# Performance work log

Measured on AMD Instinct MI355X. Metric: run time of the kernel, lower is better.

## Reference

```python
import jax, jax.numpy as jnp
import numpy as np

NUM_EMBEDDINGS = 2048
EMBEDDING_DIM = 64
COMMITMENT_COST = 0.25


def setup_inputs() -> dict:
    key = jax.random.key(0)
    k_z, k_w = jax.random.split(key)
    z = jax.random.normal(k_z, (32, EMBEDDING_DIM, 64, 64), dtype=jnp.float32)
    # torch init: uniform(-1/K, 1/K)
    embedding_w = jax.random.uniform(
        k_w, (NUM_EMBEDDINGS, EMBEDDING_DIM), dtype=jnp.float32,
        minval=-1.0 / NUM_EMBEDDINGS, maxval=1.0 / NUM_EMBEDDINGS)
    return {"z": z, "embedding_w": embedding_w}


def reference(z, embedding_w):
    # z: (B, C, H, W), C == embedding_dim
    B, C, H, W = z.shape
    zp = jnp.transpose(z, (0, 2, 3, 1))          # (B, H, W, C)
    zf = zp.reshape(-1, C)                        # (N, C)
    # squared L2 distance to every codebook entry: (N, K)
    d = (jnp.sum(zf * zf, axis=1, keepdims=True)
         + jnp.sum(embedding_w * embedding_w, axis=1)
         - 2.0 * jnp.matmul(zf, embedding_w.T))
    indices = jnp.argmin(d, axis=1)               # (N,) int
    quantized = embedding_w[indices].reshape(zp.shape)  # (B, H, W, C)
    # training-mode commitment loss: cc * mse(stop_grad(q), z)
    loss = COMMITMENT_COST * jnp.mean(
        (jax.lax.stop_gradient(quantized) - zp) ** 2)
    # straight-through estimator
    quantized_st = zp + jax.lax.stop_gradient(quantized - zp)
    quantized_out = jnp.transpose(quantized_st, (0, 3, 1, 2))  # (B, C, H, W)
    return quantized_out, indices.reshape(B, H, W), loss
```

## Files before the change

kernel.cpp:

```cpp
#include <hip/hip_runtime.h>


#define KCODES   2048
#define CDIM     64
#define OUT_Q    0
#define OUT_IDX  8388608
#define OUT_LOSS 8519680
#define ZSTR     72
#define CAP      32
#define B_MAX    1.6e-5f

typedef float f2    __attribute__((ext_vector_type(2)));
typedef float f32x4 __attribute__((ext_vector_type(4)));
typedef short s16x8 __attribute__((ext_vector_type(8)));
typedef unsigned long long u64;
typedef unsigned short u16;
typedef unsigned int u32;

__device__ __forceinline__ u16 f2bf(float x) {
    u32 u = __float_as_uint(x);
    return (u16)((u + 0x7fffu + ((u >> 16) & 1u)) >> 16);
}
__device__ __forceinline__ u32 encf(float f) {
    u32 b = __float_as_uint(f);
    return (b & 0x80000000u) ? ~b : (b | 0x80000000u);
}
__device__ __forceinline__ float decf(u32 e) {
    return __uint_as_float((e & 0x80000000u) ? (e ^ 0x80000000u) : ~e);
}

__device__ __forceinline__ float fc(const float4& v, int i) {
    return i == 0 ? v.x : (i == 1 ? v.y : (i == 2 ? v.z : v.w));
}

__device__ __forceinline__ float pairwise64(const float a[64]) {
    float r[8];
#pragma unroll
    for (int j = 0; j < 8; ++j) r[j] = a[j];
#pragma unroll
    for (int m = 1; m < 8; ++m)
#pragma unroll
        for (int j = 0; j < 8; ++j) r[j] = __fadd_rn(r[j], a[m * 8 + j]);
    float s01 = __fadd_rn(r[0], r[1]);
    float s23 = __fadd_rn(r[2], r[3]);
    float s45 = __fadd_rn(r[4], r[5]);
    float s67 = __fadd_rn(r[6], r[7]);
    return __fadd_rn(__fadd_rn(s01, s23), __fadd_rn(s45, s67));
}

__device__ __forceinline__ float exact_d(const float* __restrict__ zp,
                                         const float* __restrict__ wk,
                                         float Sr, float bk) {
    float acc = 0.f;
#pragma unroll
    for (int c0 = 0; c0 < 64; c0 += 4) {
        const float4 wc = *(const float4*)(wk + c0);
        acc = __builtin_fmaf(zp[(size_t)(c0 + 0) * 4096], wc.x, acc);
        acc = __builtin_fmaf(zp[(size_t)(c0 + 1) * 4096], wc.y, acc);
        acc = __builtin_fmaf(zp[(size_t)(c0 + 2) * 4096], wc.z, acc);
        acc = __builtin_fmaf(zp[(size_t)(c0 + 3) * 4096], wc.w, acc);
    }
    float Sb = __fadd_rn(Sr, bk);
    return __builtin_fmaf(acc, -2.0f, Sb);
}

__global__ __launch_bounds__(256) void vq_bsum(const float* __restrict__ w,
                                               float* __restrict__ bsum,
                                               u16* __restrict__ wf0,
                                               u16* __restrict__ wf1) {
    int k = blockIdx.x * 256 + threadIdx.x;
    const float4* wr = (const float4*)(w + (size_t)k * CDIM);
    float4 v[16];
    float a[64];
#pragma unroll
    for (int m = 0; m < 16; ++m) {
        v[m] = wr[m];
        a[4 * m + 0] = __fmul_rn(v[m].x, v[m].x);
        a[4 * m + 1] = __fmul_rn(v[m].y, v[m].y);
        a[4 * m + 2] = __fmul_rn(v[m].z, v[m].z);
        a[4 * m + 3] = __fmul_rn(v[m].w, v[m].w);
    }
    bsum[k] = pairwise64(a);

    const int g = k >> 4, i16 = k & 15;
#pragma unroll
    for (int h = 0; h < 2; ++h) {
        u16* wf = h ? wf1 : wf0;
#pragma unroll
        for (int o = 0; o < 4; ++o) {
            float4 va = v[h * 8 + o * 2];
            float4 vb = v[h * 8 + o * 2 + 1];
            u64 p0 = (u64)f2bf(va.x) | ((u64)f2bf(va.y) << 16)
                   | ((u64)f2bf(va.z) << 32) | ((u64)f2bf(va.w) << 48);
            u64 p1 = (u64)f2bf(vb.x) | ((u64)f2bf(vb.y) << 16)
                   | ((u64)f2bf(vb.z) << 32) | ((u64)f2bf(vb.w) << 48);
            u64* dst = (u64*)(wf + (size_t)(g * 64 + o * 16 + i16) * 8);
            dst[0] = p0; dst[1] = p1;
        }
    }
}

__global__ __launch_bounds__(256, 4) void vq_main(const float* __restrict__ z,
                                                  const float* __restrict__ w,
                                                  const float* __restrict__ bsum,
                                                  const u16* __restrict__ wf0,
                                                  const u16* __restrict__ wf1,
                                                  float* __restrict__ out,
                                                  double* __restrict__ partial) {
    __shared__ u16 zsh[64 * ZSTR];
    __shared__ float Ssh[64];
    __shared__ u32 rowmin[64];
    __shared__ float thr[64];
    __shared__ u64 skey[64];
    __shared__ u32 cnt[64];
    __shared__ u16 cand[64][CAP];
    __shared__ double lredd[4];

    const int t  = threadIdx.x;
    const int l  = t & 63;
    const int wv = t >> 6;
    const int bb = blockIdx.x;
    const size_t zbase = (size_t)(bb >> 6) * 262144 + (size_t)(bb & 63) * 64;

    if (t < 64) {
        skey[t]   = 0xFFFFFFFFFFFFFFFFull;
        cnt[t]    = 0u;
        rowmin[t] = 0xFFFFFFFFu;
    }

#pragma unroll
    for (int m = 0; m < 8; ++m) {
        int i = m * 256 + t;
        int p = i & 31;
        int c = i >> 5;
        f2 v = *(const f2*)(z + zbase + (size_t)c * 4096 + 2 * p);
        zsh[(2 * p)     * ZSTR + c] = f2bf(v.x);
        zsh[(2 * p + 1) * ZSTR + c] = f2bf(v.y);
    }

    if (t < 64) {
        const float* zp = z + zbase + t;
        float r[8];
#pragma unroll
        for (int j = 0; j < 8; ++j) {
            float v = zp[(size_t)j * 4096];
            r[j] = __fmul_rn(v, v);
        }
#pragma unroll
        for (int m = 1; m < 8; ++m)
#pragma unroll
            for (int j = 0; j < 8; ++j) {
                float v = zp[(size_t)(m * 8 + j) * 4096];
                r[j] = __fadd_rn(r[j], __fmul_rn(v, v));
            }
        float s01 = __fadd_rn(r[0], r[1]);
        float s23 = __fadd_rn(r[2], r[3]);
        float s45 = __fadd_rn(r[4], r[5]);
        float s67 = __fadd_rn(r[6], r[7]);
        Ssh[t] = __fadd_rn(__fadd_rn(s01, s23), __fadd_rn(s45, s67));
    }
    __syncthreads();

    s16x8 afrag[4][2];
#pragma unroll
    for (int mt = 0; mt < 4; ++mt)
#pragma unroll
        for (int kb = 0; kb < 2; ++kb)
            afrag[mt][kb] = *(const s16x8*)&zsh[(mt * 16 + (l & 15)) * ZSTR
                                               + kb * 32 + (l >> 4) * 8];

    const int gbase = __builtin_amdgcn_readfirstlane(wv) * 32;

    float rmin[4][4];
#pragma unroll
    for (int mt = 0; mt < 4; ++mt)
#pragma unroll
        for (int rg = 0; rg < 4; ++rg) rmin[mt][rg] = __builtin_inff();

    {
        s16x8 nb0 = *(const s16x8*)(wf0 + (size_t)(gbase * 64 + l) * 8);
        s16x8 nb1 = *(const s16x8*)(wf1 + (size_t)(gbase * 64 + l) * 8);
        float nbv = bsum[gbase * 16 + (l & 15)];
        for (int g2 = 0; g2 < 32; ++g2) {
            s16x8 b0 = nb0, b1 = nb1;
            float bv = nbv;
            if (g2 < 31) {
                int gn = gbase + g2 + 1;
                nb0 = *(const s16x8*)(wf0 + (size_t)(gn * 64 + l) * 8);
                nb1 = *(const s16x8*)(wf1 + (size_t)(gn * 64 + l) * 8);
                nbv = bsum[gn * 16 + (l & 15)];
            }
#pragma unroll
            for (int mt = 0; mt < 4; ++mt) {
                f32x4 acc = {0.f, 0.f, 0.f, 0.f};
                acc = __builtin_amdgcn_mfma_f32_16x16x32_bf16(afrag[mt][0], b0, acc, 0, 0, 0);
                acc = __builtin_amdgcn_mfma_f32_16x16x32_bf16(afrag[mt][1], b1, acc, 0, 0, 0);
#pragma unroll
                for (int rg = 0; rg < 4; ++rg) {
                    float v = __builtin_fmaf(acc[rg], -2.0f, bv);
                    rmin[mt][rg] = fminf(rmin[mt][rg], v);
                }
            }
        }
    }

#pragma unroll
    for (int mt = 0; mt < 4; ++mt)
#pragma unroll
        for (int rg = 0; rg < 4; ++rg) {
            float m = rmin[mt][rg];
            m = fminf(m, __shfl_xor(m, 1, 64));
            m = fminf(m, __shfl_xor(m, 2, 64));
            m = fminf(m, __shfl_xor(m, 4, 64));
            m = fminf(m, __shfl_xor(m, 8, 64));
            if ((l & 15) == 0)
                atomicMin(&rowmin[mt * 16 + (l >> 4) * 4 + rg], encf(m));
        }
    __syncthreads();

    if (t < 64) {
        float S = Ssh[t];
        thr[t] = decf(rowmin[t])
               + (0.03125f * sqrtf(S * B_MAX) + 7.6294e-6f * (S + 1.0f));
    }
    __syncthreads();

    float thrr[4][4];
#pragma unroll
    for (int mt = 0; mt < 4; ++mt)
#pragma unroll
        for (int rg = 0; rg < 4; ++rg)
            thrr[mt][rg] = thr[mt * 16 + (l >> 4) * 4 + rg];

    {
        s16x8 nb0 = *(const s16x8*)(wf0 + (size_t)(gbase * 64 + l) * 8);
        s16x8 nb1 = *(const s16x8*)(wf1 + (size_t)(gbase * 64 + l) * 8);
        float nbv = bsum[gbase * 16 + (l & 15)];
        for (int g2 = 0; g2 < 32; ++g2) {
            const int g = gbase + g2;
            s16x8 b0 = nb0, b1 = nb1;
            float bv = nbv;
            if (g2 < 31) {
                int gn = g + 1;
                nb0 = *(const s16x8*)(wf0 + (size_t)(gn * 64 + l) * 8);
                nb1 = *(const s16x8*)(wf1 + (size_t)(gn * 64 + l) * 8);
                nbv = bsum[gn * 16 + (l & 15)];
            }
#pragma unroll
            for (int mt = 0; mt < 4; ++mt) {
                f32x4 acc = {0.f, 0.f, 0.f, 0.f};
                acc = __builtin_amdgcn_mfma_f32_16x16x32_bf16(afrag[mt][0], b0, acc, 0, 0, 0);
                acc = __builtin_amdgcn_mfma_f32_16x16x32_bf16(afrag[mt][1], b1, acc, 0, 0, 0);
#pragma unroll
                for (int rg = 0; rg < 4; ++rg) {
                    float v = __builtin_fmaf(acc[rg], -2.0f, bv);
                    if (v <= thrr[mt][rg]) {
                        int row = mt * 16 + (l >> 4) * 4 + rg;
                        u32 pos = atomicAdd(&cnt[row], 1u);
                        if (pos < CAP)
                            cand[row][pos] = (u16)(g * 16 + (l & 15));
                    }
                }
            }
        }
    }
    __syncthreads();

    {
        const int row  = t & 63;
        const int part = t >> 6;
        const float* zp = z + zbase + row;
        const float Sr = Ssh[row];
        u32 n = cnt[row];
        if (n <= CAP) {
            for (u32 i = part; i < n; i += 4) {
                int k = cand[row][i];
                float d = exact_d(zp, w + (size_t)k * CDIM, Sr, bsum[k]);
                atomicMin(&skey[row], ((u64)__float_as_uint(d) << 32) | (u64)(u32)k);
            }
        } else {
            for (int k = part; k < KCODES; k += 4) {
                float d = exact_d(zp, w + (size_t)k * CDIM, Sr, bsum[k]);
                atomicMin(&skey[row], ((u64)__float_as_uint(d) << 32) | (u64)(u32)k);
            }
        }
    }
    __syncthreads();

    {
        const int row = l;
        const u32 kq = (u32)(skey[row] & 0xFFFFFFFFull);
        if (wv == 0) out[OUT_IDX + (size_t)bb * 64 + row] = (float)kq;

        const float* wq = w + (size_t)kq * CDIM + wv * 16;
        const float* zp = z + zbase + row;
        double lacc = 0.0;
#pragma unroll
        for (int c4 = 0; c4 < 16; c4 += 4) {
            const float4 q4 = *(const float4*)(wq + c4);
#pragma unroll
            for (int i = 0; i < 4; ++i) {
                int c = wv * 16 + c4 + i;
                float zv = zp[(size_t)c * 4096];
                float d1  = __fsub_rn(fc(q4, i), zv);
                float val = __fadd_rn(zv, d1);
                out[OUT_Q + zbase + (size_t)c * 4096 + row] = val;
                lacc += (double)__fmul_rn(d1, d1);
            }
        }
#pragma unroll
        for (int off = 1; off < 64; off <<= 1) lacc += __shfl_xor(lacc, off, 64);
        if (l == 0) lredd[wv] = lacc;
    }
    __syncthreads();
    if (t == 0) partial[bb] = lredd[0] + lredd[1] + lredd[2] + lredd[3];
}

__global__ __launch_bounds__(256) void vq_loss(const double* __restrict__ partial,
                                               float* __restrict__ out) {
    int t = threadIdx.x;
    double s = 0.0;
#pragma unroll
    for (int i = 0; i < 8; ++i) s += partial[t + i * 256];
#pragma unroll
    for (int off = 1; off < 64; off <<= 1) s += __shfl_xor(s, off, 64);
    __shared__ double sr[4];
    if ((t & 63) == 0) sr[t >> 6] = s;
    __syncthreads();
    if (t == 0)
        out[OUT_LOSS] = (float)((sr[0] + sr[1] + sr[2] + sr[3]) * (0.25 / 8388608.0));
}

extern "C" void kernel_launch(void* const* d_in, const int* in_sizes, int n_in,
                              void* d_out, int out_size, void* d_ws, size_t ws_size,
                              hipStream_t stream) {
    (void)in_sizes; (void)n_in; (void)out_size; (void)ws_size;
    const float* z = (const float*)d_in[0];
    const float* w = (const float*)d_in[1];
    float* out     = (float*)d_out;

    float*  bsum    = (float*)d_ws;
    u16*    wf0     = (u16*)((char*)d_ws + 8192);
    u16*    wf1     = (u16*)((char*)d_ws + 8192 + 131072);
    double* partial = (double*)((char*)d_ws + 8192 + 262144);

    vq_bsum<<<8, 256, 0, stream>>>(w, bsum, wf0, wf1);
    vq_main<<<2048, 256, 0, stream>>>(z, w, bsum, wf0, wf1, out, partial);
    vq_loss<<<1, 256, 0, stream>>>(partial, out);
}
```

Baseline: 190.0 us.

## Halve rows per block to 32 and fold -2 scale and bias into MFMA

Each block now handles 32 spatial rows instead of 64, so twice as many blocks are launched and every block streams the full bf16 codebook for half as many rows. The z fragments are pre-scaled by -2 and the MFMA accumulator is seeded with the codebook norm, which removes the per-element FMA before the min and threshold checks. The candidate-rescoring and output stages are remapped to 8 parts per row. The change trades codebook reuse per block (twice the codebook traffic from cache) for more parallelism and lower register use. The -2 scaling before bf16 rounding is exact and leaves the filter bounds unchanged.

```diff
diff --git a/kernel.cpp b/kernel.cpp
--- a/kernel.cpp
+++ b/kernel.cpp
@@ -7,6 +7,7 @@
 #define OUT_IDX  8388608
 #define OUT_LOSS 8519680
 #define ZSTR     72
+#define BR       32
 #define CAP      32
 #define B_MAX    1.6e-5f
 
@@ -107,38 +108,38 @@
                                                   const u16* __restrict__ wf1,
                                                   float* __restrict__ out,
                                                   double* __restrict__ partial) {
-    __shared__ u16 zsh[64 * ZSTR];
-    __shared__ float Ssh[64];
-    __shared__ u32 rowmin[64];
-    __shared__ float thr[64];
-    __shared__ u64 skey[64];
-    __shared__ u32 cnt[64];
-    __shared__ u16 cand[64][CAP];
+    __shared__ u16 zsh[BR * ZSTR];
+    __shared__ float Ssh[BR];
+    __shared__ u32 rowmin[BR];
+    __shared__ float thr[BR];
+    __shared__ u64 skey[BR];
+    __shared__ u32 cnt[BR];
+    __shared__ u16 cand[BR][CAP];
     __shared__ double lredd[4];
 
     const int t  = threadIdx.x;
     const int l  = t & 63;
     const int wv = t >> 6;
     const int bb = blockIdx.x;
-    const size_t zbase = (size_t)(bb >> 6) * 262144 + (size_t)(bb & 63) * 64;
-
-    if (t < 64) {
+    const size_t zbase = (size_t)(bb >> 7) * 262144 + (size_t)(bb & 127) * 32;
+
+    if (t < BR) {
         skey[t]   = 0xFFFFFFFFFFFFFFFFull;
         cnt[t]    = 0u;
         rowmin[t] = 0xFFFFFFFFu;
     }
 
 #pragma unroll
-    for (int m = 0; m < 8; ++m) {
+    for (int m = 0; m < 4; ++m) {
         int i = m * 256 + t;
-        int p = i & 31;
-        int c = i >> 5;
+        int p = i & 15;
+        int c = i >> 4;
         f2 v = *(const f2*)(z + zbase + (size_t)c * 4096 + 2 * p);
-        zsh[(2 * p)     * ZSTR + c] = f2bf(v.x);
-        zsh[(2 * p + 1) * ZSTR + c] = f2bf(v.y);
-    }
-
-    if (t < 64) {
+        zsh[(2 * p)     * ZSTR + c] = f2bf(-2.0f * v.x);
+        zsh[(2 * p + 1) * ZSTR + c] = f2bf(-2.0f * v.y);
+    }
+
+    if (t < BR) {
         const float* zp = z + zbase + t;
         float r[8];
 #pragma unroll
@@ -161,9 +162,9 @@
     }
     __syncthreads();
 
-    s16x8 afrag[4][2];
-#pragma unroll
-    for (int mt = 0; mt < 4; ++mt)
+    s16x8 afrag[2][2];
+#pragma unroll
+    for (int mt = 0; mt < 2; ++mt)
 #pragma unroll
         for (int kb = 0; kb < 2; ++kb)
             afrag[mt][kb] = *(const s16x8*)&zsh[(mt * 16 + (l & 15)) * ZSTR
@@ -171,9 +172,9 @@
 
     const int gbase = __builtin_amdgcn_readfirstlane(wv) * 32;
 
-    float rmin[4][4];
-#pragma unroll
-    for (int mt = 0; mt < 4; ++mt)
+    float rmin[2][4];
+#pragma unroll
+    for (int mt = 0; mt < 2; ++mt)
 #pragma unroll
         for (int rg = 0; rg < 4; ++rg) rmin[mt][rg] = __builtin_inff();
 
@@ -191,21 +192,19 @@
                 nbv = bsum[gn * 16 + (l & 15)];
             }
 #pragma unroll
-            for (int mt = 0; mt < 4; ++mt) {
-                f32x4 acc = {0.f, 0.f, 0.f, 0.f};
+            for (int mt = 0; mt < 2; ++mt) {
+                f32x4 acc = {bv, bv, bv, bv};
                 acc = __builtin_amdgcn_mfma_f32_16x16x32_bf16(afrag[mt][0], b0, acc, 0, 0, 0);
                 acc = __builtin_amdgcn_mfma_f32_16x16x32_bf16(afrag[mt][1], b1, acc, 0, 0, 0);
 #pragma unroll
-                for (int rg = 0; rg < 4; ++rg) {
-                    float v = __builtin_fmaf(acc[rg], -2.0f, bv);
-                    rmin[mt][rg] = fminf(rmin[mt][rg], v);
-                }
-            }
-        }
-    }
-
-#pragma unroll
-    for (int mt = 0; mt < 4; ++mt)
+                for (int rg = 0; rg < 4; ++rg)
+                    rmin[mt][rg] = fminf(rmin[mt][rg], acc[rg]);
+            }
+        }
+    }
+
+#pragma unroll
+    for (int mt = 0; mt < 2; ++mt)
 #pragma unroll
         for (int rg = 0; rg < 4; ++rg) {
             float m = rmin[mt][rg];
@@ -218,16 +217,16 @@
         }
     __syncthreads();
 
-    if (t < 64) {
+    if (t < BR) {
         float S = Ssh[t];
         thr[t] = decf(rowmin[t])
                + (0.03125f * sqrtf(S * B_MAX) + 7.6294e-6f * (S + 1.0f));
     }
     __syncthreads();
 
-    float thrr[4][4];
-#pragma unroll
-    for (int mt = 0; mt < 4; ++mt)
+    float thrr[2][4];
+#pragma unroll
+    for (int mt = 0; mt < 2; ++mt)
 #pragma unroll
         for (int rg = 0; rg < 4; ++rg)
             thrr[mt][rg] = thr[mt * 16 + (l >> 4) * 4 + rg];
@@ -247,14 +246,13 @@
                 nbv = bsum[gn * 16 + (l & 15)];
             }
 #pragma unroll
-            for (int mt = 0; mt < 4; ++mt) {
-                f32x4 acc = {0.f, 0.f, 0.f, 0.f};
+            for (int mt = 0; mt < 2; ++mt) {
+                f32x4 acc = {bv, bv, bv, bv};
                 acc = __builtin_amdgcn_mfma_f32_16x16x32_bf16(afrag[mt][0], b0, acc, 0, 0, 0);
                 acc = __builtin_amdgcn_mfma_f32_16x16x32_bf16(afrag[mt][1], b1, acc, 0, 0, 0);
 #pragma unroll
                 for (int rg = 0; rg < 4; ++rg) {
-                    float v = __builtin_fmaf(acc[rg], -2.0f, bv);
-                    if (v <= thrr[mt][rg]) {
+                    if (acc[rg] <= thrr[mt][rg]) {
                         int row = mt * 16 + (l >> 4) * 4 + rg;
                         u32 pos = atomicAdd(&cnt[row], 1u);
                         if (pos < CAP)
@@ -267,19 +265,19 @@
     __syncthreads();
 
     {
-        const int row  = t & 63;
-        const int part = t >> 6;
+        const int row  = t & (BR - 1);
+        const int part = t >> 5;
         const float* zp = z + zbase + row;
         const float Sr = Ssh[row];
         u32 n = cnt[row];
         if (n <= CAP) {
-            for (u32 i = part; i < n; i += 4) {
+            for (u32 i = part; i < n; i += 8) {
                 int k = cand[row][i];
                 float d = exact_d(zp, w + (size_t)k * CDIM, Sr, bsum[k]);
                 atomicMin(&skey[row], ((u64)__float_as_uint(d) << 32) | (u64)(u32)k);
             }
         } else {
-            for (int k = part; k < KCODES; k += 4) {
+            for (int k = part; k < KCODES; k += 8) {
                 float d = exact_d(zp, w + (size_t)k * CDIM, Sr, bsum[k]);
                 atomicMin(&skey[row], ((u64)__float_as_uint(d) << 32) | (u64)(u32)k);
             }
@@ -288,19 +286,20 @@
     __syncthreads();
 
     {
-        const int row = l;
+        const int row   = t & (BR - 1);
+        const int chunk = t >> 5;
         const u32 kq = (u32)(skey[row] & 0xFFFFFFFFull);
-        if (wv == 0) out[OUT_IDX + (size_t)bb * 64 + row] = (float)kq;
-
-        const float* wq = w + (size_t)kq * CDIM + wv * 16;
+        if (chunk == 0) out[OUT_IDX + (size_t)bb * BR + row] = (float)kq;
+
+        const float* wq = w + (size_t)kq * CDIM + chunk * 8;
         const float* zp = z + zbase + row;
         double lacc = 0.0;
 #pragma unroll
-        for (int c4 = 0; c4 < 16; c4 += 4) {
+        for (int c4 = 0; c4 < 8; c4 += 4) {
             const float4 q4 = *(const float4*)(wq + c4);
 #pragma unroll
             for (int i = 0; i < 4; ++i) {
-                int c = wv * 16 + c4 + i;
+                int c = chunk * 8 + c4 + i;
                 float zv = zp[(size_t)c * 4096];
                 float d1  = __fsub_rn(fc(q4, i), zv);
                 float val = __fadd_rn(zv, d1);
@@ -321,7 +320,7 @@
     int t = threadIdx.x;
     double s = 0.0;
 #pragma unroll
-    for (int i = 0; i < 8; ++i) s += partial[t + i * 256];
+    for (int i = 0; i < 16; ++i) s += partial[t + i * 256];
 #pragma unroll
     for (int off = 1; off < 64; off <<= 1) s += __shfl_xor(s, off, 64);
     __shared__ double sr[4];
@@ -345,6 +344,6 @@
     double* partial = (double*)((char*)d_ws + 8192 + 262144);
 
     vq_bsum<<<8, 256, 0, stream>>>(w, bsum, wf0, wf1);
-    vq_main<<<2048, 256, 0, stream>>>(z, w, bsum, wf0, wf1, out, partial);
+    vq_main<<<4096, 256, 0, stream>>>(z, w, bsum, wf0, wf1, out, partial);
     vq_loss<<<1, 256, 0, stream>>>(partial, out);
 }
```

After: 585.6 us. +208.2%, slower.
